# Kernel tuning notes

Measured on AMD Instinct MI355X. Metric: run time of the kernel, lower is better.

The kernel has to match this reference:

```python
import jax, jax.numpy as jnp
import numpy as np

N_DELTA, N_THETA, N_GAMMA = 64, 128, 512
N_TOTAL = N_DELTA + N_THETA + N_GAMMA  # 704
N_CLASSES = 1000
N_STEPS = 5
DT = 0.01
COUPLING = 2.0      # coupling_strength
PAC_DT = 0.3        # delta->theta phase-amplitude coupling depth
PAC_TG = 0.3        # theta->gamma phase-amplitude coupling depth
SPARSITY = 0.1      # PhaseToRateConverter sparsity (fraction of active units)
SHARP = 10.0        # softness of the 'soft' sparsification gate
TWO_PI = 2.0 * np.pi
B = 65536


def setup_inputs() -> dict:
    key = jax.random.key(0)
    k1, k2, k3, k4 = jax.random.split(key, 4)
    x = jax.random.normal(k1, (B, N_TOTAL), dtype=jnp.float32)
    # per-sample random initial phases in [0,1), scaled to [0,2pi) inside reference
    phase0 = jax.random.uniform(k2, (B, N_TOTAL), dtype=jnp.float32)
    W = jax.random.normal(k3, (N_CLASSES, N_TOTAL), dtype=jnp.float32) * 0.02
    b = jax.random.normal(k4, (N_CLASSES,), dtype=jnp.float32) * 0.02
    return {"x": x, "phase0": phase0, "W": W, "b": b}


def _kuramoto(phi):
    # mean-field within-band Kuramoto coupling: K * mean_j sin(phi_j - phi_i)
    S = jnp.mean(jnp.sin(phi), axis=-1, keepdims=True)
    C = jnp.mean(jnp.cos(phi), axis=-1, keepdims=True)
    return COUPLING * (S * jnp.cos(phi) - C * jnp.sin(phi))


def _mean_phase(phi):
    # circular mean phase of a band, shape (B,1)
    return jnp.arctan2(jnp.mean(jnp.sin(phi), axis=-1, keepdims=True),
                       jnp.mean(jnp.cos(phi), axis=-1, keepdims=True))


def _forward(x, phase0, W, b):
    freqs = jnp.concatenate([
        jnp.linspace(1.0, 4.0, N_DELTA),    # delta band Hz
        jnp.linspace(4.0, 8.0, N_THETA),    # theta band Hz
        jnp.linspace(30.0, 80.0, N_GAMMA),  # gamma band Hz
    ]).astype(x.dtype)
    phi = phase0 * TWO_PI                       # (B, N_TOTAL)
    amp = 1.0 + jnp.abs(x) * 0.01               # amplitude seeded by |x|*0.01 on unit base
    d = slice(0, N_DELTA)
    t = slice(N_DELTA, N_DELTA + N_THETA)
    g = slice(N_DELTA + N_THETA, N_TOTAL)

    def step(carry, _):
        phi, amp = carry
        dphi = TWO_PI * freqs + jnp.concatenate(
            [_kuramoto(phi[:, d]), _kuramoto(phi[:, t]), _kuramoto(phi[:, g])], axis=-1)
        psi_d = _mean_phase(phi[:, d])
        psi_t = _mean_phase(phi[:, t])
        # PAC: theta amplitude driven by delta phase, gamma amplitude by theta phase
        damp = jnp.concatenate([
            jnp.zeros_like(amp[:, d]),
            PAC_DT * amp[:, t] * jnp.cos(psi_d),
            PAC_TG * amp[:, g] * jnp.cos(psi_t),
        ], axis=-1)
        phi_new = jnp.mod(phi + DT * dphi, TWO_PI)
        amp_new = amp + DT * damp
        return (phi_new, amp_new), None

    (phi, amp), _ = jax.lax.scan(step, (phi, amp), None, length=N_STEPS)

    # PhaseToRateConverter, mode='soft': raw rate then soft top-(sparsity) gate
    raw = amp * 0.5 * (1.0 + jnp.cos(phi))                              # (B, N_TOTAL)
    thr = jnp.quantile(raw, 1.0 - SPARSITY, axis=-1, keepdims=True)    # per-sample threshold
    rate = raw * jax.nn.sigmoid((raw - thr) * SHARP)
    return rate @ W.T + b                                               # (B, N_CLASSES)


def reference(x, phase0, W, b):
    return _forward(x, phase0, W, b)
```

## Files before the change

### kernel.cpp

```cpp
#include <hip/hip_runtime.h>

#define NB 65536
#define NTOT 704
#define NCLS 1000
#define NPAD 1024
#define KDIM 704

typedef __attribute__((ext_vector_type(8))) short bf16x8;
typedef __attribute__((ext_vector_type(4))) float f32x4;
typedef __attribute__((ext_vector_type(2))) float f32x2;

#define WB_ELEMS (NPAD * KDIM)

__device__ __forceinline__ f32x2 sp(float x) { return (f32x2){x, x}; }

template <int CTRL>
__device__ __forceinline__ float dpp_shuf(float v) {
  return __int_as_float(__builtin_amdgcn_update_dpp(0, __float_as_int(v), CTRL, 0xF, 0xF, true));
}
__device__ __forceinline__ float swz16(float v) {
  return __int_as_float(__builtin_amdgcn_ds_swizzle(__float_as_int(v), 0x401F));
}
__device__ __forceinline__ float wsum_f(float v) {
  v += dpp_shuf<0xB1>(v);
  v += dpp_shuf<0x4E>(v);
  v += dpp_shuf<0x141>(v);
  v += dpp_shuf<0x140>(v);
  v += swz16(v);
  v += __shfl_xor(v, 32, 64);
  return v;
}
__device__ __forceinline__ float wmax_f(float v) {
  v = fmaxf(v, dpp_shuf<0xB1>(v));
  v = fmaxf(v, dpp_shuf<0x4E>(v));
  v = fmaxf(v, dpp_shuf<0x141>(v));
  v = fmaxf(v, dpp_shuf<0x140>(v));
  v = fmaxf(v, swz16(v));
  v = fmaxf(v, __shfl_xor(v, 32, 64));
  return v;
}
__device__ __forceinline__ float wmin_f(float v) {
  v = fminf(v, dpp_shuf<0xB1>(v));
  v = fminf(v, dpp_shuf<0x4E>(v));
  v = fminf(v, dpp_shuf<0x141>(v));
  v = fminf(v, dpp_shuf<0x140>(v));
  v = fminf(v, swz16(v));
  v = fminf(v, __shfl_xor(v, 32, 64));
  return v;
}

__device__ __forceinline__ unsigned short f2bf(float v) {
  unsigned u = __float_as_uint(v);
  u = (u + 0x7FFFu + ((u >> 16) & 1u)) >> 16;
  return (unsigned short)u;
}

__device__ __forceinline__ float freq_of(int i) {
  if (i < 64)       return 1.0f + 3.0f * (float)i * (1.0f / 63.0f);
  else if (i < 192) return 4.0f + 4.0f * (float)(i - 64) * (1.0f / 127.0f);
  else              return 30.0f + 50.0f * (float)(i - 192) * (1.0f / 511.0f);
}

__global__ __launch_bounds__(256) void sim_kernel(const float* __restrict__ x,
                                                  const float* __restrict__ p0,
                                                  const float* __restrict__ W,
                                                  unsigned short* __restrict__ Wb,
                                                  unsigned short* __restrict__ rateb) {
  {
    const int gid = blockIdx.x * 256 + threadIdx.x;
    if (gid < NPAD * KDIM) {
      const int n = gid / KDIM;
      Wb[gid] = f2bf((n < NCLS) ? W[gid] : 0.0f);
    }
  }

  const int wave = threadIdx.x >> 6;
  const int lane = threadIdx.x & 63;
  const int sample = blockIdx.x * 4 + wave;
  const size_t base = (size_t)sample * NTOT;

  float sD, cD, ampD, dcD, dsD;
  f32x2 sPp[5], cPp[5], dc2[5], ds2[5], amp2[5];
  {
    const float p = p0[base + lane];
    sD = __builtin_amdgcn_sinf(p);
    cD = __builtin_amdgcn_cosf(p);
    ampD = fmaf(fabsf(x[base + lane]), 0.01f, 1.0f);
    const float rev = 0.01f * freq_of(lane);
    dcD = __builtin_amdgcn_cosf(rev);
    dsD = __builtin_amdgcn_sinf(rev);
  }
#pragma unroll
  for (int pr = 0; pr < 5; ++pr) {
    const int i0 = (1 + 2 * pr) * 64 + lane;
    const int i1 = i0 + 64;
    const float pa = p0[base + i0], pb = p0[base + i1];
    sPp[pr] = (f32x2){__builtin_amdgcn_sinf(pa), __builtin_amdgcn_sinf(pb)};
    cPp[pr] = (f32x2){__builtin_amdgcn_cosf(pa), __builtin_amdgcn_cosf(pb)};
    amp2[pr] = (f32x2){fmaf(fabsf(x[base + i0]), 0.01f, 1.0f),
                       fmaf(fabsf(x[base + i1]), 0.01f, 1.0f)};
    const float r0 = 0.01f * freq_of(i0);
    const float r1 = 0.01f * freq_of(i1);
    dc2[pr] = (f32x2){__builtin_amdgcn_cosf(r0), __builtin_amdgcn_cosf(r1)};
    ds2[pr] = (f32x2){__builtin_amdgcn_sinf(r0), __builtin_amdgcn_sinf(r1)};
  }

  float prodT = 1.0f, prodG = 1.0f;

#pragma unroll
  for (int st = 0; st < 5; ++st) {
    const float Sd = wsum_f(sD);
    const float Cd = wsum_f(cD);
    const float St = wsum_f(sPp[0].x + sPp[0].y);
    const float Ct = wsum_f(cPp[0].x + cPp[0].y);
    const f32x2 gs = (sPp[1] + sPp[2]) + (sPp[3] + sPp[4]);
    const f32x2 gc = (cPp[1] + cPp[2]) + (cPp[3] + cPp[4]);
    const float Sg = wsum_f(gs.x + gs.y);
    const float Cg = wsum_f(gc.x + gc.y);
    const float cpd = Cd * __builtin_amdgcn_rsqf(fmaf(Sd, Sd, Cd * Cd));
    const float cpt = Ct * __builtin_amdgcn_rsqf(fmaf(St, St, Ct * Ct));
    prodT *= fmaf(0.003f, cpd, 1.0f);
    prodG *= fmaf(0.003f, cpt, 1.0f);
    const float sdm = Sd * (0.02f / 64.0f),  cdm = Cd * (0.02f / 64.0f);
    const float stm = St * (0.02f / 128.0f), ctm = Ct * (0.02f / 128.0f);
    const float sgm = Sg * (0.02f / 512.0f), cgm = Cg * (0.02f / 512.0f);
    {
      const float eps = fmaf(-cdm, sD, sdm * cD);
      const float cd_ = fmaf(-dsD, eps, dcD);
      const float sd_ = fmaf(dcD, eps, dsD);
      const float sn = fmaf(cD, sd_, sD * cd_);
      const float cn = fmaf(-sD, sd_, cD * cd_);
      sD = sn; cD = cn;
    }
#pragma unroll
    for (int pr = 0; pr < 5; ++pr) {
      const f32x2 Sm = sp(pr == 0 ? stm : sgm);
      const f32x2 Cm = sp(pr == 0 ? ctm : cgm);
      const f32x2 s2 = sPp[pr], c2 = cPp[pr];
      const f32x2 eps = Sm * c2 - Cm * s2;
      const f32x2 cosd = dc2[pr] - ds2[pr] * eps;
      const f32x2 sind = ds2[pr] + dc2[pr] * eps;
      sPp[pr] = s2 * cosd + c2 * sind;
      cPp[pr] = c2 * cosd - s2 * sind;
    }
  }

  float raw[11];
  unsigned kk[11];
  {
    const float h = 0.5f * ampD;
    raw[0] = fmaf(h, cD, h);
  }
  const float hT = 0.5f * prodT, hG = 0.5f * prodG;
#pragma unroll
  for (int pr = 0; pr < 5; ++pr) {
    const f32x2 h2 = amp2[pr] * sp(pr == 0 ? hT : hG);
    const f32x2 r2 = h2 * cPp[pr] + h2;
    raw[1 + 2 * pr] = r2.x;
    raw[2 + 2 * pr] = r2.y;
  }
#pragma unroll
  for (int e = 0; e < 11; ++e) kk[e] = (unsigned)(raw[e] * 8192.0f);

  unsigned pre = 0;
#pragma unroll
  for (int bit = 13; bit >= 0; --bit) {
    const unsigned u = pre | ((1u << bit) - 1u);
    int cnt = 0;
#pragma unroll
    for (int e = 0; e < 11; ++e) cnt += (int)__popcll(__ballot(kk[e] <= u));
    if (cnt < 633) pre |= (1u << bit);
  }

  int clt = 0, ceq = 0;
#pragma unroll
  for (int e = 0; e < 11; ++e) {
    clt += (int)__popcll(__ballot(kk[e] < pre));
    ceq += (int)__popcll(__ballot(kk[e] == pre));
  }

  const float qv = 0.9f * 703.0f;
  float thr;
  if (clt + ceq >= 634) {
    thr = ((float)pre + 0.5f) * (1.0f / 8192.0f);
  } else {
    float mx = -1.0f, mn = 3.0e38f;
#pragma unroll
    for (int e = 0; e < 11; ++e) {
      mx = fmaxf(mx, (kk[e] == pre) ? raw[e] : -1.0f);
      mn = fminf(mn, (kk[e] > pre) ? raw[e] : 3.0e38f);
    }
    const float S632 = wmax_f(mx);
    const float S633 = wmin_f(mn);
    thr = S632 * (633.0f - qv) + S633 * (qv - 632.0f);
  }

#pragma unroll
  for (int e = 0; e < 11; ++e) {
    const float r = raw[e];
    const float t = __expf((thr - r) * 10.0f);
    const float sg = __builtin_amdgcn_rcpf(1.0f + t);
    rateb[base + e * 64 + lane] = f2bf(r * sg);
  }
}

#define BK3 64
#define NK3 (KDIM / BK3)

#define FENCE __builtin_amdgcn_sched_barrier(0)
#define BAR   do { FENCE; __builtin_amdgcn_s_barrier(); FENCE; } while (0)
#define WVM8  do { asm volatile("s_waitcnt vmcnt(8)"); FENCE; } while (0)
#define WVM0  do { asm volatile("s_waitcnt vmcnt(0)"); FENCE; } while (0)
#define WLG0  do { asm volatile("s_waitcnt lgkmcnt(0)"); FENCE; } while (0)

__device__ __forceinline__ void gload16(const unsigned short* g, unsigned short* l) {
  __builtin_amdgcn_global_load_lds((const __attribute__((address_space(1))) void*)g,
                                   (__attribute__((address_space(3))) void*)l,
                                   16, 0, 0);
}

__global__ __launch_bounds__(512, 2) void gemm_kernel(const unsigned short* __restrict__ A,
                                                      const unsigned short* __restrict__ Bw,
                                                      const float* __restrict__ bias,
                                                      float* __restrict__ C) {
  __shared__ __align__(16) unsigned short lsA[4 * 8192];
  __shared__ __align__(16) unsigned short lsB[4 * 8192];
  const int tid  = threadIdx.x;
  const int wave = tid >> 6;
  const int lane = tid & 63;

  const int bid = blockIdx.x;
  const int swz = (bid & 7) * 128 + (bid >> 3);
  const int bm = swz >> 2;
  const int bn = swz & 3;

  const int wr = wave >> 2;
  const int wc = wave & 3;

  f32x4 acc[8][4];
#pragma unroll
  for (int i = 0; i < 8; ++i)
#pragma unroll
    for (int j = 0; j < 4; ++j) acc[i][j] = (f32x4){0.f, 0.f, 0.f, 0.f};

  const int srow = tid >> 3;
  const int sc16 = ((tid & 7) ^ (srow & 7)) * 8;
  const unsigned short* Ab = A  + (size_t)(bm * 256) * KDIM;
  const unsigned short* Bb = Bw + (size_t)(bn * 256) * KDIM;

#define SHALF(dst, srcb, rb, k0)                                                      \
  gload16((srcb) + (size_t)((rb) + srow) * KDIM + (k0) + sc16, (dst) + tid * 8);      \
  gload16((srcb) + (size_t)((rb) + 64 + srow) * KDIM + (k0) + sc16, (dst) + 4096 + tid * 8);

  SHALF(lsA + 0 * 8192, Ab, 0, 0)
  SHALF(lsA + 1 * 8192, Ab, 128, 0)
  SHALF(lsB + 0 * 8192, Bb, 0, 0)
  SHALF(lsB + 1 * 8192, Bb, 128, 0)
  SHALF(lsA + 2 * 8192, Ab, 0, BK3)
  SHALF(lsA + 3 * 8192, Ab, 128, BK3)
  SHALF(lsB + 2 * 8192, Bb, 0, BK3)
  SHALF(lsB + 3 * 8192, Bb, 128, BK3)

  const int l15 = lane & 15;
  const int kq  = lane >> 4;

  bf16x8 af[4][2];
  bf16x8 bg[4][2];

#pragma unroll 1
  for (int t = 0; t < NK3; ++t) {
    const int d = t & 1;
    const int k2 = (t + 2) * BK3;
    const bool stg = (t + 2) < NK3;
    const unsigned short* hA = lsA + (d * 2 + wr) * 8192;
    const unsigned short* hB = lsB + (d * 2 + (wc >> 1)) * 8192;
    const int rB0 = (wc & 1) * 64;

    if (t == NK3 - 1) { WVM0; } else { WVM8; }
    BAR;
#pragma unroll
    for (int m = 0; m < 4; ++m) {
      const int lr = m * 16 + l15;
      af[m][0] = *(const bf16x8*)&hA[lr * 64 + ((kq ^ (lr & 7)) * 8)];
      af[m][1] = *(const bf16x8*)&hA[lr * 64 + (((kq + 4) ^ (lr & 7)) * 8)];
    }
#pragma unroll
    for (int n = 0; n < 2; ++n) {
      const int lr = rB0 + n * 16 + l15;
      bg[n][0] = *(const bf16x8*)&hB[lr * 64 + ((kq ^ (lr & 7)) * 8)];
      bg[n][1] = *(const bf16x8*)&hB[lr * 64 + (((kq + 4) ^ (lr & 7)) * 8)];
    }
    WLG0;
    __builtin_amdgcn_s_setprio(1);
#pragma unroll
    for (int m = 0; m < 4; ++m)
#pragma unroll
      for (int n = 0; n < 2; ++n) {
        acc[m][n] = __builtin_amdgcn_mfma_f32_16x16x32_bf16(af[m][0], bg[n][0], acc[m][n], 0, 0, 0);
        acc[m][n] = __builtin_amdgcn_mfma_f32_16x16x32_bf16(af[m][1], bg[n][1], acc[m][n], 0, 0, 0);
      }
    __builtin_amdgcn_s_setprio(0);
    FENCE;

#pragma unroll
    for (int n = 2; n < 4; ++n) {
      const int lr = rB0 + n * 16 + l15;
      bg[n][0] = *(const bf16x8*)&hB[lr * 64 + ((kq ^ (lr & 7)) * 8)];
      bg[n][1] = *(const bf16x8*)&hB[lr * 64 + (((kq + 4) ^ (lr & 7)) * 8)];
    }
    WLG0;
    BAR;
    if (stg) {
      SHALF(lsB + (d * 2 + 0) * 8192, Bb, 0, k2)
      SHALF(lsB + (d * 2 + 1) * 8192, Bb, 128, k2)
    }
    FENCE;
    __builtin_amdgcn_s_setprio(1);
#pragma unroll
    for (int m = 0; m < 4; ++m)
#pragma unroll
      for (int n = 2; n < 4; ++n) {
        acc[m][n] = __builtin_amdgcn_mfma_f32_16x16x32_bf16(af[m][0], bg[n][0], acc[m][n], 0, 0, 0);
        acc[m][n] = __builtin_amdgcn_mfma_f32_16x16x32_bf16(af[m][1], bg[n][1], acc[m][n], 0, 0, 0);
      }
    __builtin_amdgcn_s_setprio(0);
    FENCE;

#pragma unroll
    for (int m = 0; m < 4; ++m) {
      const int lr = (m + 4) * 16 + l15;
      af[m][0] = *(const bf16x8*)&hA[lr * 64 + ((kq ^ (lr & 7)) * 8)];
      af[m][1] = *(const bf16x8*)&hA[lr * 64 + (((kq + 4) ^ (lr & 7)) * 8)];
    }
    WLG0;
    BAR;
    if (stg) {
      SHALF(lsA + (d * 2 + 0) * 8192, Ab, 0, k2)
      SHALF(lsA + (d * 2 + 1) * 8192, Ab, 128, k2)
    }
    FENCE;
    __builtin_amdgcn_s_setprio(1);
#pragma unroll
    for (int m = 0; m < 4; ++m)
#pragma unroll
      for (int n = 0; n < 2; ++n) {
        acc[m + 4][n] = __builtin_amdgcn_mfma_f32_16x16x32_bf16(af[m][0], bg[n][0], acc[m + 4][n], 0, 0, 0);
        acc[m + 4][n] = __builtin_amdgcn_mfma_f32_16x16x32_bf16(af[m][1], bg[n][1], acc[m + 4][n], 0, 0, 0);
      }
    __builtin_amdgcn_s_setprio(0);
    FENCE;

    __builtin_amdgcn_s_setprio(1);
#pragma unroll
    for (int m = 0; m < 4; ++m)
#pragma unroll
      for (int n = 2; n < 4; ++n) {
        acc[m + 4][n] = __builtin_amdgcn_mfma_f32_16x16x32_bf16(af[m][0], bg[n][0], acc[m + 4][n], 0, 0, 0);
        acc[m + 4][n] = __builtin_amdgcn_mfma_f32_16x16x32_bf16(af[m][1], bg[n][1], acc[m + 4][n], 0, 0, 0);
      }
    __builtin_amdgcn_s_setprio(0);
    FENCE;
  }

  const int crow0 = bm * 256 + wr * 128;
  const int ccol0 = bn * 256 + wc * 64;
  const int rql = (lane >> 4) * 4;
  const int cl  = lane & 15;
#pragma unroll
  for (int n = 0; n < 4; ++n) {
    const int col = ccol0 + n * 16 + cl;
    if (col < NCLS) {
      const float bb = bias[col];
#pragma unroll
      for (int m = 0; m < 8; ++m) {
#pragma unroll
        for (int r = 0; r < 4; ++r) {
          const int row = crow0 + m * 16 + rql + r;
          C[(size_t)row * NCLS + col] = acc[m][n][r] + bb;
        }
      }
    }
  }
}

extern "C" void kernel_launch(void* const* d_in, const int* in_sizes, int n_in,
                              void* d_out, int out_size, void* d_ws, size_t ws_size,
                              hipStream_t stream) {
  const float* x    = (const float*)d_in[0];
  const float* p0   = (const float*)d_in[1];
  const float* W    = (const float*)d_in[2];
  const float* bias = (const float*)d_in[3];
  float* out = (float*)d_out;

  unsigned short* Wb    = (unsigned short*)d_ws;
  unsigned short* rateb = (unsigned short*)d_ws + WB_ELEMS;

  sim_kernel<<<dim3(NB / 4), dim3(256), 0, stream>>>(x, p0, W, Wb, rateb);
  gemm_kernel<<<dim3((NB / 256) * (NPAD / 256)), dim3(512), 0, stream>>>(rateb, Wb, bias, out);
}
```

Baseline: 293.9 us.

## Halve GEMM K-tile to 32 and raise occupancy to four blocks per CU

Shrinks the GEMM K-step from 64 to 32, which halves the LDS staging buffers and fragment registers. The per-step global-to-LDS loads, the XOR swizzle pattern and the vmcnt wait are reworked to match. Launch bounds now ask for 4 blocks per CU so more waves can hide latency. The cost is twice as many loop iterations and barriers per tile. Register pressure from the 128-float accumulator may block the higher occupancy and cause spills.

```diff
diff --git a/kernel.cpp b/kernel.cpp
--- a/kernel.cpp
+++ b/kernel.cpp
@@ -204,12 +204,12 @@
   }
 }
 
-#define BK3 64
+#define BK3 32
 #define NK3 (KDIM / BK3)
 
 #define FENCE __builtin_amdgcn_sched_barrier(0)
 #define BAR   do { FENCE; __builtin_amdgcn_s_barrier(); FENCE; } while (0)
-#define WVM8  do { asm volatile("s_waitcnt vmcnt(8)"); FENCE; } while (0)
+#define WVM4  do { asm volatile("s_waitcnt vmcnt(4)"); FENCE; } while (0)
 #define WVM0  do { asm volatile("s_waitcnt vmcnt(0)"); FENCE; } while (0)
 #define WLG0  do { asm volatile("s_waitcnt lgkmcnt(0)"); FENCE; } while (0)
 
@@ -219,12 +219,12 @@
                                    16, 0, 0);
 }
 
-__global__ __launch_bounds__(512, 2) void gemm_kernel(const unsigned short* __restrict__ A,
+__global__ __launch_bounds__(512, 4) void gemm_kernel(const unsigned short* __restrict__ A,
                                                       const unsigned short* __restrict__ Bw,
                                                       const float* __restrict__ bias,
                                                       float* __restrict__ C) {
-  __shared__ __align__(16) unsigned short lsA[4 * 8192];
-  __shared__ __align__(16) unsigned short lsB[4 * 8192];
+  __shared__ __align__(16) unsigned short lsA[2 * 8192];
+  __shared__ __align__(16) unsigned short lsB[2 * 8192];
   const int tid  = threadIdx.x;
   const int wave = tid >> 6;
   const int lane = tid & 63;
@@ -243,110 +243,90 @@
 #pragma unroll
     for (int j = 0; j < 4; ++j) acc[i][j] = (f32x4){0.f, 0.f, 0.f, 0.f};
 
-  const int srow = tid >> 3;
-  const int sc16 = ((tid & 7) ^ (srow & 7)) * 8;
+  const int srow4 = tid >> 2;
+  const int ksrc  = (((tid & 3) ^ ((tid >> 3) & 3))) * 8;
   const unsigned short* Ab = A  + (size_t)(bm * 256) * KDIM;
   const unsigned short* Bb = Bw + (size_t)(bn * 256) * KDIM;
 
-#define SHALF(dst, srcb, rb, k0)                                                      \
-  gload16((srcb) + (size_t)((rb) + srow) * KDIM + (k0) + sc16, (dst) + tid * 8);      \
-  gload16((srcb) + (size_t)((rb) + 64 + srow) * KDIM + (k0) + sc16, (dst) + 4096 + tid * 8);
-
-  SHALF(lsA + 0 * 8192, Ab, 0, 0)
-  SHALF(lsA + 1 * 8192, Ab, 128, 0)
-  SHALF(lsB + 0 * 8192, Bb, 0, 0)
-  SHALF(lsB + 1 * 8192, Bb, 128, 0)
-  SHALF(lsA + 2 * 8192, Ab, 0, BK3)
-  SHALF(lsA + 3 * 8192, Ab, 128, BK3)
-  SHALF(lsB + 2 * 8192, Bb, 0, BK3)
-  SHALF(lsB + 3 * 8192, Bb, 128, BK3)
+#define SOP32(dst, srcb, k0)                                                          \
+  gload16((srcb) + (size_t)(srow4) * KDIM + (k0) + ksrc, (dst) + tid * 8);            \
+  gload16((srcb) + (size_t)(128 + srow4) * KDIM + (k0) + ksrc, (dst) + 4096 + tid * 8);
+
+  SOP32(lsA + 0 * 8192, Ab, 0)
+  SOP32(lsB + 0 * 8192, Bb, 0)
+  SOP32(lsA + 1 * 8192, Ab, BK3)
+  SOP32(lsB + 1 * 8192, Bb, BK3)
 
   const int l15 = lane & 15;
   const int kq  = lane >> 4;
 
-  bf16x8 af[4][2];
-  bf16x8 bg[4][2];
+  bf16x8 af[4];
+  bf16x8 bg[4];
 
 #pragma unroll 1
   for (int t = 0; t < NK3; ++t) {
     const int d = t & 1;
     const int k2 = (t + 2) * BK3;
     const bool stg = (t + 2) < NK3;
-    const unsigned short* hA = lsA + (d * 2 + wr) * 8192;
-    const unsigned short* hB = lsB + (d * 2 + (wc >> 1)) * 8192;
+    const unsigned short* hA = lsA + d * 8192 + wr * 4096;
+    const unsigned short* hB = lsB + d * 8192 + (wc >> 1) * 4096;
     const int rB0 = (wc & 1) * 64;
 
-    if (t == NK3 - 1) { WVM0; } else { WVM8; }
+    if (t == NK3 - 1) { WVM0; } else { WVM4; }
     BAR;
 #pragma unroll
     for (int m = 0; m < 4; ++m) {
       const int lr = m * 16 + l15;
-      af[m][0] = *(const bf16x8*)&hA[lr * 64 + ((kq ^ (lr & 7)) * 8)];
-      af[m][1] = *(const bf16x8*)&hA[lr * 64 + (((kq + 4) ^ (lr & 7)) * 8)];
+      af[m] = *(const bf16x8*)&hA[lr * 32 + ((kq ^ ((lr >> 1) & 3)) * 8)];
     }
 #pragma unroll
     for (int n = 0; n < 2; ++n) {
       const int lr = rB0 + n * 16 + l15;
-      bg[n][0] = *(const bf16x8*)&hB[lr * 64 + ((kq ^ (lr & 7)) * 8)];
-      bg[n][1] = *(const bf16x8*)&hB[lr * 64 + (((kq + 4) ^ (lr & 7)) * 8)];
+      bg[n] = *(const bf16x8*)&hB[lr * 32 + ((kq ^ ((lr >> 1) & 3)) * 8)];
     }
     WLG0;
     __builtin_amdgcn_s_setprio(1);
 #pragma unroll
     for (int m = 0; m < 4; ++m)
 #pragma unroll
-      for (int n = 0; n < 2; ++n) {
-        acc[m][n] = __builtin_amdgcn_mfma_f32_16x16x32_bf16(af[m][0], bg[n][0], acc[m][n], 0, 0, 0);
-        acc[m][n] = __builtin_amdgcn_mfma_f32_16x16x32_bf16(af[m][1], bg[n][1], acc[m][n], 0, 0, 0);
-      }
+      for (int n = 0; n < 2; ++n)
+        acc[m][n] = __builtin_amdgcn_mfma_f32_16x16x32_bf16(af[m], bg[n], acc[m][n], 0, 0, 0);
     __builtin_amdgcn_s_setprio(0);
     FENCE;
 
 #pragma unroll
     for (int n = 2; n < 4; ++n) {
       const int lr = rB0 + n * 16 + l15;
-      bg[n][0] = *(const bf16x8*)&hB[lr * 64 + ((kq ^ (lr & 7)) * 8)];
-      bg[n][1] = *(const bf16x8*)&hB[lr * 64 + (((kq + 4) ^ (lr & 7)) * 8)];
+      bg[n] = *(const bf16x8*)&hB[lr * 32 + ((kq ^ ((lr >> 1) & 3)) * 8)];
     }
     WLG0;
     BAR;
-    if (stg) {
-      SHALF(lsB + (d * 2 + 0) * 8192, Bb, 0, k2)
-      SHALF(lsB + (d * 2 + 1) * 8192, Bb, 128, k2)
-    }
+    if (stg) { SOP32(lsB + d * 8192, Bb, k2) }
     FENCE;
     __builtin_amdgcn_s_setprio(1);
 #pragma unroll
     for (int m = 0; m < 4; ++m)
 #pragma unroll
-      for (int n = 2; n < 4; ++n) {
-        acc[m][n] = __builtin_amdgcn_mfma_f32_16x16x32_bf16(af[m][0], bg[n][0], acc[m][n], 0, 0, 0);
-        acc[m][n] = __builtin_amdgcn_mfma_f32_16x16x32_bf16(af[m][1], bg[n][1], acc[m][n], 0, 0, 0);
-      }
+      for (int n = 2; n < 4; ++n)
+        acc[m][n] = __builtin_amdgcn_mfma_f32_16x16x32_bf16(af[m], bg[n], acc[m][n], 0, 0, 0);
     __builtin_amdgcn_s_setprio(0);
     FENCE;
 
 #pragma unroll
     for (int m = 0; m < 4; ++m) {
       const int lr = (m + 4) * 16 + l15;
-      af[m][0] = *(const bf16x8*)&hA[lr * 64 + ((kq ^ (lr & 7)) * 8)];
-      af[m][1] = *(const bf16x8*)&hA[lr * 64 + (((kq + 4) ^ (lr & 7)) * 8)];
+      af[m] = *(const bf16x8*)&hA[lr * 32 + ((kq ^ ((lr >> 1) & 3)) * 8)];
     }
     WLG0;
     BAR;
-    if (stg) {
-      SHALF(lsA + (d * 2 + 0) * 8192, Ab, 0, k2)
-      SHALF(lsA + (d * 2 + 1) * 8192, Ab, 128, k2)
-    }
+    if (stg) { SOP32(lsA + d * 8192, Ab, k2) }
     FENCE;
     __builtin_amdgcn_s_setprio(1);
 #pragma unroll
     for (int m = 0; m < 4; ++m)
 #pragma unroll
-      for (int n = 0; n < 2; ++n) {
-        acc[m + 4][n] = __builtin_amdgcn_mfma_f32_16x16x32_bf16(af[m][0], bg[n][0], acc[m + 4][n], 0, 0, 0);
-        acc[m + 4][n] = __builtin_amdgcn_mfma_f32_16x16x32_bf16(af[m][1], bg[n][1], acc[m + 4][n], 0, 0, 0);
-      }
+      for (int n = 0; n < 2; ++n)
+        acc[m + 4][n] = __builtin_amdgcn_mfma_f32_16x16x32_bf16(af[m], bg[n], acc[m + 4][n], 0, 0, 0);
     __builtin_amdgcn_s_setprio(0);
     FENCE;
 
@@ -354,10 +334,8 @@
 #pragma unroll
     for (int m = 0; m < 4; ++m)
 #pragma unroll
-      for (int n = 2; n < 4; ++n) {
-        acc[m + 4][n] = __builtin_amdgcn_mfma_f32_16x16x32_bf16(af[m][0], bg[n][0], acc[m + 4][n], 0, 0, 0);
-        acc[m + 4][n] = __builtin_amdgcn_mfma_f32_16x16x32_bf16(af[m][1], bg[n][1], acc[m + 4][n], 0, 0, 0);
-      }
+      for (int n = 2; n < 4; ++n)
+        acc[m + 4][n] = __builtin_amdgcn_mfma_f32_16x16x32_bf16(af[m], bg[n], acc[m + 4][n], 0, 0, 0);
     __builtin_amdgcn_s_setprio(0);
     FENCE;
   }
```

Measured after the change: 948.7 us. 223% more time.
